# Kernel optimization log

Measured on AMD Instinct MI355X. Metric: run time of the kernel, lower is better.

The kernel has to match this reference:

```python
import jax, jax.numpy as jnp
import numpy as np

DIM = 1024
N_SRC = 4096
N_TGT = 4096


def setup_inputs() -> dict:
    key = jax.random.key(0)
    ks = jax.random.split(key, 7)
    scale = 1.0 / np.sqrt(DIM)
    return {
        "source": jax.random.normal(ks[0], (N_SRC, DIM), dtype=jnp.float32),
        "target": jax.random.normal(ks[1], (N_TGT, DIM), dtype=jnp.float32),
        "W_src": jax.random.uniform(ks[2], (DIM, DIM), minval=-scale, maxval=scale, dtype=jnp.float32),
        "b_src": jax.random.uniform(ks[3], (DIM,), minval=-scale, maxval=scale, dtype=jnp.float32),
        "W_tgt": jax.random.uniform(ks[4], (DIM, DIM), minval=-scale, maxval=scale, dtype=jnp.float32),
        "b_tgt": jax.random.uniform(ks[5], (DIM,), minval=-scale, maxval=scale, dtype=jnp.float32),
        "temperature": jnp.array(1.0, dtype=jnp.float32),
    }


def reference(source, target, W_src, b_src, W_tgt, b_tgt, temperature):
    # Linear projections (torch Linear: x @ W.T + b)
    sp = source @ W_src.T + b_src            # [N, d]
    tp = target @ W_tgt.T + b_tgt            # [M, d]
    sq_s = jnp.sum(sp * sp, axis=-1, keepdims=True)   # [N, 1]
    sq_t = jnp.sum(tp * tp, axis=-1)                  # [M]
    d2 = sq_s + sq_t[None, :] - 2.0 * (sp @ tp.T)     # [N, M]
    cost = jnp.sqrt(jnp.maximum(d2, 0.0))
    # Softmin-style kernel, row-normalized over target entries
    K = jnp.exp(-cost / temperature)
    K = K / jnp.sum(K, axis=1, keepdims=True)
    aligned_source = K @ target                       # [N, d]
    return aligned_source, K
```

## Files before the change

kernel.cpp:

```cpp
#include <hip/hip_runtime.h>
#include <stdint.h>

#define DIM  1024
#define NSRC 4096
#define NTGT 4096

typedef __bf16 bf16_t;
typedef bf16_t bf16x8 __attribute__((ext_vector_type(8)));
typedef float  fx4    __attribute__((ext_vector_type(4)));

static __device__ __forceinline__ unsigned short f2bf(float f) {
  union { float f; uint32_t u; } v; v.f = f;
  return (unsigned short)((v.u + 0x7FFFu + ((v.u >> 16) & 1u)) >> 16);
}
static __device__ __forceinline__ float bf2f(unsigned short h) {
  union { uint32_t u; float f; } v; v.u = ((uint32_t)h) << 16;
  return v.f;
}

static __device__ __forceinline__ void gl_lds16(const unsigned short* g, unsigned short* l) {
  __builtin_amdgcn_global_load_lds(
      (__attribute__((address_space(1))) const void*)g,
      (__attribute__((address_space(3))) void*)l, 16, 0, 0);
}

typedef const __attribute__((address_space(3))) unsigned short* lds3p;

template <int IMM>
static __device__ __forceinline__ bf16x8 dsr128(lds3p p) {
  bf16x8 r;
  asm volatile("ds_read_b128 %0, %1 offset:%2" : "=v"(r) : "v"(p), "n"(IMM));
  return r;
}


__global__ void k_convert_all(const float* __restrict__ s, const float* __restrict__ t,
                              const float* __restrict__ w0, const float* __restrict__ w1,
                              unsigned short* __restrict__ sb, unsigned short* __restrict__ tb,
                              unsigned short* __restrict__ wb0, unsigned short* __restrict__ wb1) {
  int b = blockIdx.x;
  const float* in; unsigned short* out; int idx;
  if (b < 4096)      { in = s;  out = sb;  idx = b * 256 + threadIdx.x; }
  else if (b < 8192) { in = t;  out = tb;  idx = (b - 4096) * 256 + threadIdx.x; }
  else if (b < 9216) { in = w0; out = wb0; idx = (b - 8192) * 256 + threadIdx.x; }
  else               { in = w1; out = wb1; idx = (b - 9216) * 256 + threadIdx.x; }
  float4 v = ((const float4*)in)[idx];
  ushort4 o;
  o.x = f2bf(v.x); o.y = f2bf(v.y); o.z = f2bf(v.z); o.w = f2bf(v.w);
  ((ushort4*)out)[idx] = o;
}

__global__ void k_transpose_bf16(const float* __restrict__ in, unsigned short* __restrict__ out,
                                 int R, int C) {
  __shared__ unsigned short tile[32][33];
  int c0 = blockIdx.x * 32, r0 = blockIdx.y * 32;
  int tx = threadIdx.x, ty = threadIdx.y;
  for (int i = ty; i < 32; i += 8) {
    int row = r0 + i;
    int p = row & 63;
    int tr = (row & ~63) | ((p >> 2) | ((p & 3) << 4));
    tile[i][tx] = f2bf(in[(size_t)tr * C + c0 + tx]);
  }
  __syncthreads();
  for (int i = ty; i < 32; i += 8)
    out[(size_t)(c0 + i) * R + r0 + tx] = tile[tx][i];
}

__global__ void k_finalize_aligned(const float* __restrict__ P, float* __restrict__ aligned,
                                   const float* __restrict__ rs) {
  const int b = blockIdx.x;
  const int lane = threadIdx.x & 63, w = threadIdx.x >> 6;
  const int src = ((lane & 15) << 2) | (lane >> 4);
  const size_t stride = (size_t)NSRC * DIM;
#pragma unroll
  for (int it = 0; it < 4; ++it) {
    int idx = b * 16 + w * 4 + it;
    size_t base = (size_t)idx * 64;
    float r = 1.0f / rs[idx >> 4];
    float v = (P[base + lane] + P[base + stride + lane] +
               P[base + 2 * stride + lane] + P[base + 3 * stride + lane]) * r;
    aligned[base + lane] = __shfl(v, src, 64);
  }
}

__global__ void k_finalize_K(const unsigned short* __restrict__ Eb, float* __restrict__ Kf,
                             const float* __restrict__ rs) {
  const int b = blockIdx.x;
  const int lane = threadIdx.x & 63, w = threadIdx.x >> 6;
  const int src = ((lane & 15) << 2) | (lane >> 4);
#pragma unroll
  for (int it = 0; it < 8; ++it) {
    int idx = b * 32 + w * 8 + it;
    size_t base = (size_t)idx * 64;
    float r = 1.0f / rs[idx >> 6];
    float v = bf2f(Eb[base + lane]) * r;
    Kf[base + lane] = __shfl(v, src, 64);
  }
}

template <int EPI, int LDK>
__global__ void __launch_bounds__(512, 2)
k_tile256(const unsigned short* __restrict__ A0, const unsigned short* __restrict__ B0,
          const unsigned short* __restrict__ A1, const unsigned short* __restrict__ B1,
          const float* __restrict__ bias0, const float* __restrict__ bias1,
          unsigned short* __restrict__ Cb0, unsigned short* __restrict__ Cb1,
          unsigned short* __restrict__ Eb, float* __restrict__ Cf,
          const float* __restrict__ sqs, const float* __restrict__ sqt,
          const float* __restrict__ tempPtr,
          float* __restrict__ red0, float* __restrict__ red1) {
  __shared__ unsigned short ldsA[32768];
  __shared__ unsigned short ldsB[32768];

  const unsigned short* A = A0;
  const unsigned short* B = B0;
  const float* bias = bias0;
  unsigned short* Cb = Cb0;
  float* red = red0;
  if constexpr (EPI == 0) {
    if (blockIdx.z) { A = A1; B = B1; bias = bias1; Cb = Cb1; red = red1; }
  }
  if constexpr (EPI == 3) { A += blockIdx.z * 1024; B += blockIdx.z * 1024; }

  int nbx = blockIdx.x, nby = blockIdx.y;
  {
    const int nx = gridDim.x, n = gridDim.x * gridDim.y;
    const int id = nby * nx + nbx;
    const int q = n >> 3;
    const int s = (id & 7) * q + (id >> 3);
    nbx = s % nx; nby = s / nx;
  }

  const int tid = threadIdx.x;
  const int lane = tid & 63, w = tid >> 6;
  const int wm = w >> 2, wn = w & 3;
  const int fr = lane & 15, kq = lane >> 4;
  const int m0 = nby * 256, n0 = nbx * 256;

  const int rg = lane >> 3;
  const int sk = ((lane & 7) ^ rg) * 8;
  const size_t aS = (size_t)(m0 + w * 8 + rg) * LDK + sk;
  const size_t bS = (size_t)(n0 + w * 8 + rg) * LDK + sk;

  const int eA = fr & 7;
  const lds3p baseA0 = (lds3p)ldsA + (wm * 128 + fr) * 64 + ((kq ^ eA) * 8);
  const lds3p baseA1 = (lds3p)ldsA + (wm * 128 + fr) * 64 + (((4 + kq) ^ eA) * 8);
  const lds3p baseB0 = (lds3p)ldsB + (wn * 64 + fr) * 64 + ((kq ^ eA) * 8);
  const lds3p baseB1 = (lds3p)ldsB + (wn * 64 + fr) * 64 + (((4 + kq) ^ eA) * 8);

#define STAGE(buf, tk) do { \
    gl_lds16(A + aS + (size_t)(tk),                 ldsA + (buf) * 16384 + w * 512); \
    gl_lds16(A + aS + 64 * (size_t)LDK + (tk),      ldsA + (buf) * 16384 + 4096 + w * 512); \
    gl_lds16(A + aS + 128 * (size_t)LDK + (tk),     ldsA + (buf) * 16384 + 8192 + w * 512); \
    gl_lds16(A + aS + 192 * (size_t)LDK + (tk),     ldsA + (buf) * 16384 + 12288 + w * 512); \
    gl_lds16(B + bS + (size_t)(tk),                 ldsB + (buf) * 16384 + w * 512); \
    gl_lds16(B + bS + 64 * (size_t)LDK + (tk),      ldsB + (buf) * 16384 + 4096 + w * 512); \
    gl_lds16(B + bS + 128 * (size_t)LDK + (tk),     ldsB + (buf) * 16384 + 8192 + w * 512); \
    gl_lds16(B + bS + 192 * (size_t)LDK + (tk),     ldsB + (buf) * 16384 + 12288 + w * 512); \
  } while (0)

  const fx4 fz = {0.f, 0.f, 0.f, 0.f};
  fx4 acc[8][4];
#pragma unroll
  for (int i = 0; i < 8; ++i)
#pragma unroll
    for (int j = 0; j < 4; ++j) acc[i][j] = fz;

  bf16x8 a[8][2], b[4][2];

#define RD24(buf) do { \
    a[0][0] = dsr128<(buf) * 32768 +     0>(baseA0); \
    a[1][0] = dsr128<(buf) * 32768 +  2048>(baseA0); \
    a[2][0] = dsr128<(buf) * 32768 +  4096>(baseA0); \
    a[3][0] = dsr128<(buf) * 32768 +  6144>(baseA0); \
    a[4][0] = dsr128<(buf) * 32768 +  8192>(baseA0); \
    a[5][0] = dsr128<(buf) * 32768 + 10240>(baseA0); \
    a[6][0] = dsr128<(buf) * 32768 + 12288>(baseA0); \
    a[7][0] = dsr128<(buf) * 32768 + 14336>(baseA0); \
    a[0][1] = dsr128<(buf) * 32768 +     0>(baseA1); \
    a[1][1] = dsr128<(buf) * 32768 +  2048>(baseA1); \
    a[2][1] = dsr128<(buf) * 32768 +  4096>(baseA1); \
    a[3][1] = dsr128<(buf) * 32768 +  6144>(baseA1); \
    a[4][1] = dsr128<(buf) * 32768 +  8192>(baseA1); \
    a[5][1] = dsr128<(buf) * 32768 + 10240>(baseA1); \
    a[6][1] = dsr128<(buf) * 32768 + 12288>(baseA1); \
    a[7][1] = dsr128<(buf) * 32768 + 14336>(baseA1); \
    b[0][0] = dsr128<(buf) * 32768 +     0>(baseB0); \
    b[1][0] = dsr128<(buf) * 32768 +  2048>(baseB0); \
    b[2][0] = dsr128<(buf) * 32768 +  4096>(baseB0); \
    b[3][0] = dsr128<(buf) * 32768 +  6144>(baseB0); \
    b[0][1] = dsr128<(buf) * 32768 +     0>(baseB1); \
    b[1][1] = dsr128<(buf) * 32768 +  2048>(baseB1); \
    b[2][1] = dsr128<(buf) * 32768 +  4096>(baseB1); \
    b[3][1] = dsr128<(buf) * 32768 +  6144>(baseB1); \
  } while (0)

#define MFMA64() do { _Pragma("unroll") \
    for (int i = 0; i < 8; ++i) { _Pragma("unroll") \
      for (int j = 0; j < 4; ++j) { \
        acc[i][j] = __builtin_amdgcn_mfma_f32_16x16x32_bf16(a[i][0], b[j][0], acc[i][j], 0, 0, 0); \
        acc[i][j] = __builtin_amdgcn_mfma_f32_16x16x32_bf16(a[i][1], b[j][1], acc[i][j], 0, 0, 0); \
      } } } while (0)

#define SB0()   __builtin_amdgcn_sched_barrier(0)
#define BARS()  do { SB0(); __builtin_amdgcn_s_barrier(); SB0(); } while (0)
#define LGKM0() do { asm volatile("s_waitcnt lgkmcnt(0)" ::: "memory"); SB0(); } while (0)
#define VM8()   do { asm volatile("s_waitcnt vmcnt(8)" ::: "memory"); SB0(); } while (0)
#define VM0()   do { asm volatile("s_waitcnt vmcnt(0)" ::: "memory"); SB0(); } while (0)

#define PH_MAIN(buf, tk2) do { \
    RD24(buf); \
    LGKM0(); \
    BARS(); \
    STAGE(buf, tk2); SB0(); \
    __builtin_amdgcn_s_setprio(1); MFMA64(); __builtin_amdgcn_s_setprio(0); \
    VM8(); \
    BARS(); \
  } while (0)

  STAGE(0, 0);
  STAGE(1, 64);
  VM8();
  BARS();

#pragma unroll 1
  for (int it = 0; it < 7; ++it) {
    PH_MAIN(0, it * 128 + 128);
    PH_MAIN(1, it * 128 + 192);
  }
  RD24(0);
  LGKM0();
  BARS();
  __builtin_amdgcn_s_setprio(1); MFMA64(); __builtin_amdgcn_s_setprio(0);
  VM0();
  BARS();
  RD24(1);
  LGKM0();
  __builtin_amdgcn_s_setprio(1); MFMA64(); __builtin_amdgcn_s_setprio(0);

  const int gcol0 = n0 + wn * 64 + fr;
  const int scol  = n0 + wn * 64 + fr * 4;

  if constexpr (EPI == 0) {
#pragma unroll
    for (int i = 0; i < 8; ++i)
#pragma unroll
      for (int r = 0; r < 4; ++r) {
        const int gm = m0 + wm * 128 + i * 16 + kq * 4 + r;
        float racc = 0.f;
        ushort4 o; unsigned short* op = (unsigned short*)&o;
#pragma unroll
        for (int j = 0; j < 4; ++j) {
          float e = acc[i][j][r] + bias[gcol0 + j * 16];
          unsigned short eb = f2bf(e);
          op[j] = eb;
          float ev = bf2f(eb);
          racc += ev * ev;
        }
        *(ushort4*)(Cb + (size_t)gm * DIM + scol) = o;
        racc += __shfl_xor(racc, 1, 64);
        racc += __shfl_xor(racc, 2, 64);
        racc += __shfl_xor(racc, 4, 64);
        racc += __shfl_xor(racc, 8, 64);
        if (fr == 0) atomicAdd(&red[gm], racc);
      }
  } else if constexpr (EPI == 1) {
    const float invT = 1.0f / tempPtr[0];
#pragma unroll
    for (int i = 0; i < 8; ++i)
#pragma unroll
      for (int r = 0; r < 4; ++r) {
        const int gm = m0 + wm * 128 + i * 16 + kq * 4 + r;
        const float si = sqs[gm];
        float racc = 0.f;
        ushort4 o; unsigned short* op = (unsigned short*)&o;
#pragma unroll
        for (int j = 0; j < 4; ++j) {
          float d2 = si + sqt[gcol0 + j * 16] - 2.0f * acc[i][j][r];
          float c = sqrtf(fmaxf(d2, 0.0f));
          unsigned short eb = f2bf(__expf(-c * invT));
          op[j] = eb;
          racc += bf2f(eb);
        }
        *(ushort4*)(Eb + (size_t)gm * NTGT + scol) = o;
        racc += __shfl_xor(racc, 1, 64);
        racc += __shfl_xor(racc, 2, 64);
        racc += __shfl_xor(racc, 4, 64);
        racc += __shfl_xor(racc, 8, 64);
        if (fr == 0) atomicAdd(&red[gm], racc);
      }
  } else {
    float* Pz = Cf + (size_t)blockIdx.z * NSRC * DIM;
#pragma unroll
    for (int i = 0; i < 8; ++i)
#pragma unroll
      for (int r = 0; r < 4; ++r) {
        const int gm = m0 + wm * 128 + i * 16 + kq * 4 + r;
        float4 v = make_float4(acc[i][0][r], acc[i][1][r], acc[i][2][r], acc[i][3][r]);
        *(float4*)(Pz + (size_t)gm * DIM + scol) = v;
      }
  }
#undef STAGE
#undef RD24
#undef MFMA64
#undef PH_MAIN
#undef SB0
#undef BARS
#undef LGKM0
#undef VM8
#undef VM0
}

extern "C" void kernel_launch(void* const* d_in, const int* in_sizes, int n_in,
                              void* d_out, int out_size, void* d_ws, size_t ws_size,
                              hipStream_t stream) {
  const float* source = (const float*)d_in[0];
  const float* target = (const float*)d_in[1];
  const float* W_src  = (const float*)d_in[2];
  const float* b_src  = (const float*)d_in[3];
  const float* W_tgt  = (const float*)d_in[4];
  const float* b_tgt  = (const float*)d_in[5];
  const float* temp   = (const float*)d_in[6];

  float* out     = (float*)d_out;
  float* aligned = out;
  float* Kout    = out + (size_t)NSRC * DIM;
  float* parts   = Kout;

  char* ws = (char*)d_ws;
  unsigned short* src_b  = (unsigned short*)(ws + 0);
  unsigned short* tgt_b  = (unsigned short*)(ws + 8388608);
  unsigned short* Wsrc_b = (unsigned short*)(ws + 16777216);
  unsigned short* Wtgt_b = (unsigned short*)(ws + 18874368);
  unsigned short* sp_b   = (unsigned short*)(ws + 20971520);
  unsigned short* tp_b   = (unsigned short*)(ws + 29360128);
  unsigned short* tgtT_b = (unsigned short*)(ws + 37748736);
  unsigned short* E_b    = (unsigned short*)(ws + 46137344);
  float* sq_s  = (float*)(ws + 79691776);
  float* sq_t  = (float*)(ws + 79708160);
  float* rsums = (float*)(ws + 79724544);

  hipMemsetAsync(sq_s, 0, 3 * NSRC * sizeof(float), stream);

  k_convert_all<<<10240, 256, 0, stream>>>(source, target, W_src, W_tgt,
                                           src_b, tgt_b, Wsrc_b, Wtgt_b);
  k_transpose_bf16<<<dim3(DIM / 32, NTGT / 32), dim3(32, 8), 0, stream>>>(target, tgtT_b, NTGT, DIM);

  k_tile256<0, DIM><<<dim3(DIM / 256, NSRC / 256, 2), 512, 0, stream>>>(
      src_b, Wsrc_b, tgt_b, Wtgt_b, b_src, b_tgt, sp_b, tp_b,
      nullptr, nullptr, nullptr, nullptr, nullptr, sq_s, sq_t);

  k_tile256<1, DIM><<<dim3(NTGT / 256, NSRC / 256, 1), 512, 0, stream>>>(
      sp_b, tp_b, nullptr, nullptr, nullptr, nullptr, nullptr, nullptr,
      E_b, nullptr, sq_s, sq_t, temp, rsums, nullptr);

  k_tile256<3, NTGT><<<dim3(DIM / 256, NSRC / 256, 4), 512, 0, stream>>>(
      E_b, tgtT_b, nullptr, nullptr, nullptr, nullptr, nullptr, nullptr,
      nullptr, parts, nullptr, nullptr, nullptr, nullptr, nullptr);

  k_finalize_aligned<<<4096, 256, 0, stream>>>(parts, aligned, rsums);
  k_finalize_K<<<8192, 256, 0, stream>>>(E_b, Kout, rsums);
}
```

Measured before the change: 277.0 us.

## Switch GEMMs to 128x128 tiles with 256 threads and halve split-K

Replaces the 256x256, 512-thread GEMM tile kernel with a 128x128, 256-thread variant that uses half the LDS per block and runs a different double-buffered pipeline: each step stages the next K tile, then reads and computes the current one. The final aligned GEMM now splits K two ways instead of four, so the finalize kernel sums two partials instead of four. Smaller tiles give more blocks per GEMM (better CU fill at these sizes) and less partial-sum traffic, at the cost of lower operand reuse per block and more global/LDS loads per FLOP.

```diff
diff --git a/kernel.cpp b/kernel.cpp
--- a/kernel.cpp
+++ b/kernel.cpp
@@ -77,8 +77,7 @@
     int idx = b * 16 + w * 4 + it;
     size_t base = (size_t)idx * 64;
     float r = 1.0f / rs[idx >> 4];
-    float v = (P[base + lane] + P[base + stride + lane] +
-               P[base + 2 * stride + lane] + P[base + 3 * stride + lane]) * r;
+    float v = (P[base + lane] + P[base + stride + lane]) * r;
     aligned[base + lane] = __shfl(v, src, 64);
   }
 }
@@ -98,9 +97,9 @@
   }
 }
 
-template <int EPI, int LDK>
-__global__ void __launch_bounds__(512, 2)
-k_tile256(const unsigned short* __restrict__ A0, const unsigned short* __restrict__ B0,
+template <int EPI, int LDK, int KT>
+__global__ void __launch_bounds__(256, 2)
+k_tile128(const unsigned short* __restrict__ A0, const unsigned short* __restrict__ B0,
           const unsigned short* __restrict__ A1, const unsigned short* __restrict__ B1,
           const float* __restrict__ bias0, const float* __restrict__ bias1,
           unsigned short* __restrict__ Cb0, unsigned short* __restrict__ Cb1,
@@ -108,8 +107,8 @@
           const float* __restrict__ sqs, const float* __restrict__ sqt,
           const float* __restrict__ tempPtr,
           float* __restrict__ red0, float* __restrict__ red1) {
-  __shared__ unsigned short ldsA[32768];
-  __shared__ unsigned short ldsB[32768];
+  __shared__ unsigned short ldsA[16384];
+  __shared__ unsigned short ldsB[16384];
 
   const unsigned short* A = A0;
   const unsigned short* B = B0;
@@ -119,7 +118,7 @@
   if constexpr (EPI == 0) {
     if (blockIdx.z) { A = A1; B = B1; bias = bias1; Cb = Cb1; red = red1; }
   }
-  if constexpr (EPI == 3) { A += blockIdx.z * 1024; B += blockIdx.z * 1024; }
+  if constexpr (EPI == 3) { A += blockIdx.z * 2048; B += blockIdx.z * 2048; }
 
   int nbx = blockIdx.x, nby = blockIdx.y;
   {
@@ -132,9 +131,9 @@
 
   const int tid = threadIdx.x;
   const int lane = tid & 63, w = tid >> 6;
-  const int wm = w >> 2, wn = w & 3;
+  const int wm = w >> 1, wn = w & 1;
   const int fr = lane & 15, kq = lane >> 4;
-  const int m0 = nby * 256, n0 = nbx * 256;
+  const int m0 = nby * 128, n0 = nbx * 128;
 
   const int rg = lane >> 3;
   const int sk = ((lane & 7) ^ rg) * 8;
@@ -142,60 +141,52 @@
   const size_t bS = (size_t)(n0 + w * 8 + rg) * LDK + sk;
 
   const int eA = fr & 7;
-  const lds3p baseA0 = (lds3p)ldsA + (wm * 128 + fr) * 64 + ((kq ^ eA) * 8);
-  const lds3p baseA1 = (lds3p)ldsA + (wm * 128 + fr) * 64 + (((4 + kq) ^ eA) * 8);
+  const lds3p baseA0 = (lds3p)ldsA + (wm * 64 + fr) * 64 + ((kq ^ eA) * 8);
+  const lds3p baseA1 = (lds3p)ldsA + (wm * 64 + fr) * 64 + (((4 + kq) ^ eA) * 8);
   const lds3p baseB0 = (lds3p)ldsB + (wn * 64 + fr) * 64 + ((kq ^ eA) * 8);
   const lds3p baseB1 = (lds3p)ldsB + (wn * 64 + fr) * 64 + (((4 + kq) ^ eA) * 8);
 
 #define STAGE(buf, tk) do { \
-    gl_lds16(A + aS + (size_t)(tk),                 ldsA + (buf) * 16384 + w * 512); \
-    gl_lds16(A + aS + 64 * (size_t)LDK + (tk),      ldsA + (buf) * 16384 + 4096 + w * 512); \
-    gl_lds16(A + aS + 128 * (size_t)LDK + (tk),     ldsA + (buf) * 16384 + 8192 + w * 512); \
-    gl_lds16(A + aS + 192 * (size_t)LDK + (tk),     ldsA + (buf) * 16384 + 12288 + w * 512); \
-    gl_lds16(B + bS + (size_t)(tk),                 ldsB + (buf) * 16384 + w * 512); \
-    gl_lds16(B + bS + 64 * (size_t)LDK + (tk),      ldsB + (buf) * 16384 + 4096 + w * 512); \
-    gl_lds16(B + bS + 128 * (size_t)LDK + (tk),     ldsB + (buf) * 16384 + 8192 + w * 512); \
-    gl_lds16(B + bS + 192 * (size_t)LDK + (tk),     ldsB + (buf) * 16384 + 12288 + w * 512); \
+    gl_lds16(A + aS + (size_t)(tk),              ldsA + (buf) * 8192 + w * 512); \
+    gl_lds16(A + aS + 32 * (size_t)LDK + (tk),   ldsA + (buf) * 8192 + 2048 + w * 512); \
+    gl_lds16(A + aS + 64 * (size_t)LDK + (tk),   ldsA + (buf) * 8192 + 4096 + w * 512); \
+    gl_lds16(A + aS + 96 * (size_t)LDK + (tk),   ldsA + (buf) * 8192 + 6144 + w * 512); \
+    gl_lds16(B + bS + (size_t)(tk),              ldsB + (buf) * 8192 + w * 512); \
+    gl_lds16(B + bS + 32 * (size_t)LDK + (tk),   ldsB + (buf) * 8192 + 2048 + w * 512); \
+    gl_lds16(B + bS + 64 * (size_t)LDK + (tk),   ldsB + (buf) * 8192 + 4096 + w * 512); \
+    gl_lds16(B + bS + 96 * (size_t)LDK + (tk),   ldsB + (buf) * 8192 + 6144 + w * 512); \
   } while (0)
 
   const fx4 fz = {0.f, 0.f, 0.f, 0.f};
-  fx4 acc[8][4];
-#pragma unroll
-  for (int i = 0; i < 8; ++i)
+  fx4 acc[4][4];
+#pragma unroll
+  for (int i = 0; i < 4; ++i)
 #pragma unroll
     for (int j = 0; j < 4; ++j) acc[i][j] = fz;
 
-  bf16x8 a[8][2], b[4][2];
-
-#define RD24(buf) do { \
-    a[0][0] = dsr128<(buf) * 32768 +     0>(baseA0); \
-    a[1][0] = dsr128<(buf) * 32768 +  2048>(baseA0); \
-    a[2][0] = dsr128<(buf) * 32768 +  4096>(baseA0); \
-    a[3][0] = dsr128<(buf) * 32768 +  6144>(baseA0); \
-    a[4][0] = dsr128<(buf) * 32768 +  8192>(baseA0); \
-    a[5][0] = dsr128<(buf) * 32768 + 10240>(baseA0); \
-    a[6][0] = dsr128<(buf) * 32768 + 12288>(baseA0); \
-    a[7][0] = dsr128<(buf) * 32768 + 14336>(baseA0); \
-    a[0][1] = dsr128<(buf) * 32768 +     0>(baseA1); \
-    a[1][1] = dsr128<(buf) * 32768 +  2048>(baseA1); \
-    a[2][1] = dsr128<(buf) * 32768 +  4096>(baseA1); \
-    a[3][1] = dsr128<(buf) * 32768 +  6144>(baseA1); \
-    a[4][1] = dsr128<(buf) * 32768 +  8192>(baseA1); \
-    a[5][1] = dsr128<(buf) * 32768 + 10240>(baseA1); \
-    a[6][1] = dsr128<(buf) * 32768 + 12288>(baseA1); \
-    a[7][1] = dsr128<(buf) * 32768 + 14336>(baseA1); \
-    b[0][0] = dsr128<(buf) * 32768 +     0>(baseB0); \
-    b[1][0] = dsr128<(buf) * 32768 +  2048>(baseB0); \
-    b[2][0] = dsr128<(buf) * 32768 +  4096>(baseB0); \
-    b[3][0] = dsr128<(buf) * 32768 +  6144>(baseB0); \
-    b[0][1] = dsr128<(buf) * 32768 +     0>(baseB1); \
-    b[1][1] = dsr128<(buf) * 32768 +  2048>(baseB1); \
-    b[2][1] = dsr128<(buf) * 32768 +  4096>(baseB1); \
-    b[3][1] = dsr128<(buf) * 32768 +  6144>(baseB1); \
+  bf16x8 a[4][2], b[4][2];
+
+#define RD16(buf) do { \
+    a[0][0] = dsr128<(buf) * 16384 +    0>(baseA0); \
+    a[1][0] = dsr128<(buf) * 16384 + 2048>(baseA0); \
+    a[2][0] = dsr128<(buf) * 16384 + 4096>(baseA0); \
+    a[3][0] = dsr128<(buf) * 16384 + 6144>(baseA0); \
+    a[0][1] = dsr128<(buf) * 16384 +    0>(baseA1); \
+    a[1][1] = dsr128<(buf) * 16384 + 2048>(baseA1); \
+    a[2][1] = dsr128<(buf) * 16384 + 4096>(baseA1); \
+    a[3][1] = dsr128<(buf) * 16384 + 6144>(baseA1); \
+    b[0][0] = dsr128<(buf) * 16384 +    0>(baseB0); \
+    b[1][0] = dsr128<(buf) * 16384 + 2048>(baseB0); \
+    b[2][0] = dsr128<(buf) * 16384 + 4096>(baseB0); \
+    b[3][0] = dsr128<(buf) * 16384 + 6144>(baseB0); \
+    b[0][1] = dsr128<(buf) * 16384 +    0>(baseB1); \
+    b[1][1] = dsr128<(buf) * 16384 + 2048>(baseB1); \
+    b[2][1] = dsr128<(buf) * 16384 + 4096>(baseB1); \
+    b[3][1] = dsr128<(buf) * 16384 + 6144>(baseB1); \
   } while (0)
 
-#define MFMA64() do { _Pragma("unroll") \
-    for (int i = 0; i < 8; ++i) { _Pragma("unroll") \
+#define MFMA32() do { _Pragma("unroll") \
+    for (int i = 0; i < 4; ++i) { _Pragma("unroll") \
       for (int j = 0; j < 4; ++j) { \
         acc[i][j] = __builtin_amdgcn_mfma_f32_16x16x32_bf16(a[i][0], b[j][0], acc[i][j], 0, 0, 0); \
         acc[i][j] = __builtin_amdgcn_mfma_f32_16x16x32_bf16(a[i][1], b[j][1], acc[i][j], 0, 0, 0); \
@@ -207,45 +198,34 @@
 #define VM8()   do { asm volatile("s_waitcnt vmcnt(8)" ::: "memory"); SB0(); } while (0)
 #define VM0()   do { asm volatile("s_waitcnt vmcnt(0)" ::: "memory"); SB0(); } while (0)
 
-#define PH_MAIN(buf, tk2) do { \
-    RD24(buf); \
-    LGKM0(); \
-    BARS(); \
-    STAGE(buf, tk2); SB0(); \
-    __builtin_amdgcn_s_setprio(1); MFMA64(); __builtin_amdgcn_s_setprio(0); \
-    VM8(); \
+#define HALF(buf, nbuf, tk) do { \
+    STAGE(nbuf, tk); \
+    VM8(); BARS(); \
+    RD16(buf); LGKM0(); \
+    __builtin_amdgcn_s_setprio(1); MFMA32(); __builtin_amdgcn_s_setprio(0); \
     BARS(); \
   } while (0)
 
   STAGE(0, 0);
-  STAGE(1, 64);
-  VM8();
-  BARS();
-
 #pragma unroll 1
-  for (int it = 0; it < 7; ++it) {
-    PH_MAIN(0, it * 128 + 128);
-    PH_MAIN(1, it * 128 + 192);
-  }
-  RD24(0);
-  LGKM0();
-  BARS();
-  __builtin_amdgcn_s_setprio(1); MFMA64(); __builtin_amdgcn_s_setprio(0);
-  VM0();
-  BARS();
-  RD24(1);
-  LGKM0();
-  __builtin_amdgcn_s_setprio(1); MFMA64(); __builtin_amdgcn_s_setprio(0);
+  for (int t = 0; t < KT / 2 - 1; ++t) {
+    HALF(0, 1, (2 * t + 1) * 64);
+    HALF(1, 0, (2 * t + 2) * 64);
+  }
+  HALF(0, 1, (KT - 1) * 64);
+  VM0(); BARS();
+  RD16(1); LGKM0();
+  __builtin_amdgcn_s_setprio(1); MFMA32(); __builtin_amdgcn_s_setprio(0);
 
   const int gcol0 = n0 + wn * 64 + fr;
   const int scol  = n0 + wn * 64 + fr * 4;
 
   if constexpr (EPI == 0) {
 #pragma unroll
-    for (int i = 0; i < 8; ++i)
+    for (int i = 0; i < 4; ++i)
 #pragma unroll
       for (int r = 0; r < 4; ++r) {
-        const int gm = m0 + wm * 128 + i * 16 + kq * 4 + r;
+        const int gm = m0 + wm * 64 + i * 16 + kq * 4 + r;
         float racc = 0.f;
         ushort4 o; unsigned short* op = (unsigned short*)&o;
 #pragma unroll
@@ -266,10 +246,10 @@
   } else if constexpr (EPI == 1) {
     const float invT = 1.0f / tempPtr[0];
 #pragma unroll
-    for (int i = 0; i < 8; ++i)
+    for (int i = 0; i < 4; ++i)
 #pragma unroll
       for (int r = 0; r < 4; ++r) {
-        const int gm = m0 + wm * 128 + i * 16 + kq * 4 + r;
+        const int gm = m0 + wm * 64 + i * 16 + kq * 4 + r;
         const float si = sqs[gm];
         float racc = 0.f;
         ushort4 o; unsigned short* op = (unsigned short*)&o;
@@ -291,18 +271,18 @@
   } else {
     float* Pz = Cf + (size_t)blockIdx.z * NSRC * DIM;
 #pragma unroll
-    for (int i = 0; i < 8; ++i)
+    for (int i = 0; i < 4; ++i)
 #pragma unroll
       for (int r = 0; r < 4; ++r) {
-        const int gm = m0 + wm * 128 + i * 16 + kq * 4 + r;
+        const int gm = m0 + wm * 64 + i * 16 + kq * 4 + r;
         float4 v = make_float4(acc[i][0][r], acc[i][1][r], acc[i][2][r], acc[i][3][r]);
         *(float4*)(Pz + (size_t)gm * DIM + scol) = v;
       }
   }
 #undef STAGE
-#undef RD24
-#undef MFMA64
-#undef PH_MAIN
+#undef RD16
+#undef MFMA32
+#undef HALF
 #undef SB0
 #undef BARS
 #undef LGKM0
@@ -345,15 +325,15 @@
                                            src_b, tgt_b, Wsrc_b, Wtgt_b);
   k_transpose_bf16<<<dim3(DIM / 32, NTGT / 32), dim3(32, 8), 0, stream>>>(target, tgtT_b, NTGT, DIM);
 
-  k_tile256<0, DIM><<<dim3(DIM / 256, NSRC / 256, 2), 512, 0, stream>>>(
+  k_tile128<0, DIM, 16><<<dim3(DIM / 128, NSRC / 128, 2), 256, 0, stream>>>(
       src_b, Wsrc_b, tgt_b, Wtgt_b, b_src, b_tgt, sp_b, tp_b,
       nullptr, nullptr, nullptr, nullptr, nullptr, sq_s, sq_t);
 
-  k_tile256<1, DIM><<<dim3(NTGT / 256, NSRC / 256, 1), 512, 0, stream>>>(
+  k_tile128<1, DIM, 16><<<dim3(NTGT / 128, NSRC / 128, 1), 256, 0, stream>>>(
       sp_b, tp_b, nullptr, nullptr, nullptr, nullptr, nullptr, nullptr,
       E_b, nullptr, sq_s, sq_t, temp, rsums, nullptr);
 
-  k_tile256<3, NTGT><<<dim3(DIM / 256, NSRC / 256, 4), 512, 0, stream>>>(
+  k_tile128<3, NTGT, 32><<<dim3(DIM / 128, NSRC / 128, 2), 256, 0, stream>>>(
       E_b, tgtT_b, nullptr, nullptr, nullptr, nullptr, nullptr, nullptr,
       nullptr, parts, nullptr, nullptr, nullptr, nullptr, nullptr);
 
```

New measurement: 262.0 us. 1.06x faster.
